# Kernel tuning notes

Measured on AMD Instinct MI355X. Metric: run time of the kernel, lower is better.

Reference implementation:

```python
import jax, jax.numpy as jnp
import numpy as np

D_MODEL = 512
INF = 1e9
TEMP = np.sqrt(D_MODEL).astype(np.float32)


def setup_inputs() -> dict:
    key = jax.random.key(0)
    kq, kk, kv, km = jax.random.split(key, 4)
    B, L, D = 64, 1024, 64  # B = batch*heads
    q = jax.random.normal(kq, (B, L, D), dtype=jnp.float32)
    k = jax.random.normal(kk, (B, L, D), dtype=jnp.float32)
    v = jax.random.normal(kv, (B, L, D), dtype=jnp.float32)
    attn_mask = jax.random.randint(km, (B, L, L), 0, 2).astype(jnp.bool_)
    return {"q": q, "k": k, "v": v, "attn_mask": attn_mask}


def reference(q, k, v, attn_mask):
    # scores: [b, len_q, len_k]
    attn = jnp.einsum('bqd,bkd->bqk', q, k) / TEMP
    attn = jnp.where(attn_mask, -INF, attn)
    attn = jax.nn.softmax(attn, axis=2)
    # dropout p=0.0 -> identity
    out = jnp.einsum('bqk,bkd->bqd', attn, v)
    return out
```

## Files before the change

kernel.cpp:

```cpp
#include <hip/hip_runtime.h>
#include <hip/hip_bf16.h>


typedef __attribute__((ext_vector_type(4))) float f32x4;
typedef __attribute__((ext_vector_type(8))) short bf16x8;
typedef __attribute__((ext_vector_type(4))) short short4v;

constexpr int B_ = 64;
constexpr int L_ = 1024;
constexpr int D_ = 64;
constexpr int QBLK = 64;
constexpr int KV = 64;
constexpr int NKV = L_ / KV;
constexpr int STR = 72;
constexpr float INV_TEMP = 0.04419417382415922f;
constexpr float NEG = -1e9f;

__device__ inline short f2bf(float f) {
  __hip_bfloat16 h = __float2bfloat16(f);
  short s; __builtin_memcpy(&s, &h, 2);
  return s;
}

__global__ __launch_bounds__(256, 3) void attn_fwd(
    const float* __restrict__ Q, const float* __restrict__ K,
    const float* __restrict__ V, const int* __restrict__ M,
    float* __restrict__ O)
{
  __shared__ short k_lds[2][KV][STR];
  __shared__ short vt_lds[2][D_][STR];
  __shared__ short p_lds[4][16][STR];

  const int tid  = threadIdx.x;
  const int w    = tid >> 6;
  const int lane = tid & 63;
  const int g    = lane >> 4;
  const int c    = lane & 15;

  const int p   = blockIdx.x;
  const int xcd = p & 7;
  const int j   = p >> 3;
  const int b   = xcd + 8 * (j >> 4);
  const int q0  = (j & 15) * QBLK;

  bf16x8 qf[2];
  {
    const float* qp = Q + ((size_t)b * L_ + q0 + w * 16 + c) * D_ + g * 8;
#pragma unroll
    for (int ks = 0; ks < 2; ++ks) {
      f32x4 x0 = *(const f32x4*)(qp + ks * 32);
      f32x4 x1 = *(const f32x4*)(qp + ks * 32 + 4);
      bf16x8 t;
      t[0] = f2bf(x0[0]); t[1] = f2bf(x0[1]); t[2] = f2bf(x0[2]); t[3] = f2bf(x0[3]);
      t[4] = f2bf(x1[0]); t[5] = f2bf(x1[1]); t[6] = f2bf(x1[2]); t[7] = f2bf(x1[3]);
      qf[ks] = t;
    }
  }

  const float* Kb = K + (size_t)b * L_ * D_;
  const float* Vb = V + (size_t)b * L_ * D_;
  const int* mlane = M + (size_t)b * L_ * L_ + (size_t)(q0 + w * 16 + c) * L_ + 4 * g;

  f32x4 kreg[4], vreg[4];
  int4  mA[4], mB[4];
  const int vkey4 = (tid & 15) * 4;
  const int vd4   = (tid >> 4) * 4;

  auto load_kv = [&](int t) {
    const float* ksrc = Kb + (size_t)(t * KV) * D_;
    const float* vsrc = Vb + (size_t)(t * KV) * D_;
#pragma unroll
    for (int i = 0; i < 4; ++i) {
      kreg[i] = *(const f32x4*)(ksrc + (size_t)(tid + i * 256) * 4);
      vreg[i] = *(const f32x4*)(vsrc + (size_t)(vkey4 + i) * D_ + vd4);
    }
  };
  auto load_m = [&](int t, int4 (&mr)[4]) {
#pragma unroll
    for (int f = 0; f < 4; ++f) mr[f] = *(const int4*)(mlane + t * KV + f * 16);
  };
  auto write_kv = [&](int buf) {
#pragma unroll
    for (int i = 0; i < 4; ++i) {
      const int idx = tid + i * 256;
      short4v ks4 = { f2bf(kreg[i][0]), f2bf(kreg[i][1]),
                      f2bf(kreg[i][2]), f2bf(kreg[i][3]) };
      *(short4v*)&k_lds[buf][idx >> 4][(idx & 15) * 4] = ks4;
      const int jj = (i + (tid >> 4)) & 3;
      short4v vt4 = { f2bf(vreg[0][jj]), f2bf(vreg[1][jj]),
                      f2bf(vreg[2][jj]), f2bf(vreg[3][jj]) };
      *(short4v*)&vt_lds[buf][vd4 + jj][vkey4] = vt4;
    }
  };

  f32x4 acc[4];
#pragma unroll
  for (int i = 0; i < 4; ++i) acc[i] = (f32x4){0.f, 0.f, 0.f, 0.f};
  float m_run = -INFINITY;
  float l_run = 0.f;

  load_kv(0);
  write_kv(0);
  load_m(0, mA);
  load_m(1, mB);
  __syncthreads();

  auto body = [&](int t, int4 (&mbuf)[4], bool refill) {
    const int cur = t & 1;
    const bool has_next = (t + 1 < NKV);
    if (has_next) load_kv(t + 1);
    int4 mc[4];
#pragma unroll
    for (int f = 0; f < 4; ++f) mc[f] = mbuf[f];
    if (refill) load_m(t + 2, mbuf);
    __builtin_amdgcn_sched_barrier(0);

    f32x4 sc[4];
#pragma unroll
    for (int f = 0; f < 4; ++f) {
      f32x4 a = (f32x4){0.f, 0.f, 0.f, 0.f};
#pragma unroll
      for (int ks = 0; ks < 2; ++ks) {
        bf16x8 kf = *(const bf16x8*)&k_lds[cur][f * 16 + c][ks * 32 + g * 8];
        a = __builtin_amdgcn_mfma_f32_16x16x32_bf16(kf, qf[ks], a, 0, 0, 0);
      }
      sc[f] = a;
    }

#pragma unroll
    for (int f = 0; f < 4; ++f) {
      const int4 mm = mc[f];
      sc[f][0] = mm.x ? NEG : sc[f][0] * INV_TEMP;
      sc[f][1] = mm.y ? NEG : sc[f][1] * INV_TEMP;
      sc[f][2] = mm.z ? NEG : sc[f][2] * INV_TEMP;
      sc[f][3] = mm.w ? NEG : sc[f][3] * INV_TEMP;
    }

    float x = sc[0][0];
#pragma unroll
    for (int f = 0; f < 4; ++f)
#pragma unroll
      for (int r = 0; r < 4; ++r) x = fmaxf(x, sc[f][r]);
    x = fmaxf(x, __shfl_xor(x, 16, 64));
    x = fmaxf(x, __shfl_xor(x, 32, 64));
    const float m_new = fmaxf(m_run, x);
    const float alpha = __expf(m_run - m_new);
    float s = 0.f;
#pragma unroll
    for (int f = 0; f < 4; ++f)
#pragma unroll
      for (int r = 0; r < 4; ++r) {
        sc[f][r] = __expf(sc[f][r] - m_new);
        s += sc[f][r];
      }
    s += __shfl_xor(s, 16, 64);
    s += __shfl_xor(s, 32, 64);
    l_run = l_run * alpha + s;
    m_run = m_new;

    float ar[4];
#pragma unroll
    for (int r = 0; r < 4; ++r)
      ar[r] = __shfl(alpha, (lane & 48) | (g * 4 + r), 64);
#pragma unroll
    for (int fd = 0; fd < 4; ++fd)
#pragma unroll
      for (int r = 0; r < 4; ++r) acc[fd][r] *= ar[r];

#pragma unroll
    for (int f = 0; f < 4; ++f) {
      short4v pk = { f2bf(sc[f][0]), f2bf(sc[f][1]),
                     f2bf(sc[f][2]), f2bf(sc[f][3]) };
      *(short4v*)&p_lds[w][c][f * 16 + 4 * g] = pk;
    }

#pragma unroll
    for (int ks = 0; ks < 2; ++ks) {
      bf16x8 pa = *(const bf16x8*)&p_lds[w][c][ks * 32 + g * 8];
#pragma unroll
      for (int fd = 0; fd < 4; ++fd) {
        bf16x8 vb = *(const bf16x8*)&vt_lds[cur][fd * 16 + c][ks * 32 + g * 8];
        acc[fd] = __builtin_amdgcn_mfma_f32_16x16x32_bf16(pa, vb, acc[fd], 0, 0, 0);
      }
    }

    if (has_next) write_kv(cur ^ 1);
    __syncthreads();
  };

  for (int tt = 0; tt < NKV; tt += 2) {
    body(tt,     mA, tt + 2 < NKV);
    body(tt + 1, mB, tt + 3 < NKV);
  }

  const float li = 1.0f / l_run;
  float lr[4];
#pragma unroll
  for (int r = 0; r < 4; ++r)
    lr[r] = __shfl(li, (lane & 48) | (g * 4 + r), 64);
  float* orow = O + ((size_t)b * L_ + q0 + w * 16 + g * 4) * D_;
#pragma unroll
  for (int fd = 0; fd < 4; ++fd)
#pragma unroll
    for (int r = 0; r < 4; ++r)
      orow[(size_t)r * D_ + fd * 16 + c] = acc[fd][r] * lr[r];
}

extern "C" void kernel_launch(void* const* d_in, const int* in_sizes, int n_in,
                              void* d_out, int out_size, void* d_ws, size_t ws_size,
                              hipStream_t stream) {
  const float* q = (const float*)d_in[0];
  const float* k = (const float*)d_in[1];
  const float* v = (const float*)d_in[2];
  const int* m = (const int*)d_in[3];
  float* o = (float*)d_out;
  attn_fwd<<<dim3(1024), 256, 0, stream>>>(q, k, v, m, o);
}
```

Measured before the change: 97.46 us.

## Redistribute softmax probabilities via lane shuffles instead of LDS round-trip

```diff
diff --git a/kernel.cpp b/kernel.cpp
--- a/kernel.cpp
+++ b/kernel.cpp
@@ -21,15 +21,18 @@
   short s; __builtin_memcpy(&s, &h, 2);
   return s;
 }
-
-__global__ __launch_bounds__(256, 3) void attn_fwd(
+__device__ inline unsigned int pk2(float a, float b) {
+  return (unsigned int)(unsigned short)f2bf(a)
+       | ((unsigned int)(unsigned short)f2bf(b) << 16);
+}
+
+__global__ __launch_bounds__(256, 4) void attn_fwd(
     const float* __restrict__ Q, const float* __restrict__ K,
     const float* __restrict__ V, const int* __restrict__ M,
     float* __restrict__ O)
 {
   __shared__ short k_lds[2][KV][STR];
   __shared__ short vt_lds[2][D_][STR];
-  __shared__ short p_lds[4][16][STR];
 
   const int tid  = threadIdx.x;
   const int w    = tid >> 6;
@@ -167,21 +170,44 @@
 #pragma unroll
       for (int r = 0; r < 4; ++r) acc[fd][r] *= ar[r];
 
+    unsigned int pd[4][2];
 #pragma unroll
     for (int f = 0; f < 4; ++f) {
-      short4v pk = { f2bf(sc[f][0]), f2bf(sc[f][1]),
-                     f2bf(sc[f][2]), f2bf(sc[f][3]) };
-      *(short4v*)&p_lds[w][c][f * 16 + 4 * g] = pk;
-    }
-
-#pragma unroll
-    for (int ks = 0; ks < 2; ++ks) {
-      bf16x8 pa = *(const bf16x8*)&p_lds[w][c][ks * 32 + g * 8];
-#pragma unroll
-      for (int fd = 0; fd < 4; ++fd) {
-        bf16x8 vb = *(const bf16x8*)&vt_lds[cur][fd * 16 + c][ks * 32 + g * 8];
-        acc[fd] = __builtin_amdgcn_mfma_f32_16x16x32_bf16(pa, vb, acc[fd], 0, 0, 0);
+      pd[f][0] = pk2(sc[f][0], sc[f][1]);
+      pd[f][1] = pk2(sc[f][2], sc[f][3]);
+    }
+    const int rev2 = ((g & 1) << 1) | (g >> 1);
+    const int srcA = rev2 * 16 + c;
+    const int srcB = srcA ^ 16;
+    const bool podd = (g & 1) != 0;
+    const bool gh   = (g >= 2);
+    unsigned int d0[4], d1[4];
+#pragma unroll
+    for (int k = 0; k < 4; ++k) {
+      const int fb = 2 * (k >> 1);
+      const int hh = k & 1;
+      const unsigned int pubA = podd ? pd[fb + 1][hh] : pd[fb + 0][hh];
+      const unsigned int pubB = podd ? pd[fb + 0][hh] : pd[fb + 1][hh];
+      const unsigned int rvA = (unsigned int)__shfl((int)pubA, srcA, 64);
+      const unsigned int rvB = (unsigned int)__shfl((int)pubB, srcB, 64);
+      if (k < 2) {
+        if (gh) { d0[2 + hh] = rvA; d0[hh] = rvB; }
+        else    { d0[hh] = rvA; d0[2 + hh] = rvB; }
+      } else {
+        if (gh) { d1[2 + hh] = rvA; d1[hh] = rvB; }
+        else    { d1[hh] = rvA; d1[2 + hh] = rvB; }
       }
+    }
+    bf16x8 pa0, pa1;
+    __builtin_memcpy(&pa0, d0, 16);
+    __builtin_memcpy(&pa1, d1, 16);
+
+#pragma unroll
+    for (int fd = 0; fd < 4; ++fd) {
+      bf16x8 vb0 = *(const bf16x8*)&vt_lds[cur][fd * 16 + c][g * 8];
+      acc[fd] = __builtin_amdgcn_mfma_f32_16x16x32_bf16(pa0, vb0, acc[fd], 0, 0, 0);
+      bf16x8 vb1 = *(const bf16x8*)&vt_lds[cur][fd * 16 + c][32 + g * 8];
+      acc[fd] = __builtin_amdgcn_mfma_f32_16x16x32_bf16(pa1, vb1, acc[fd], 0, 0, 0);
     }
 
     if (has_next) write_kv(cur ^ 1);
```

After: 213.8 us. 2.19x slower.
